# Optimization experiments

Measured on AMD Instinct MI355X. Metric: run time of the kernel, lower is better.

## Reference

```python
import jax, jax.numpy as jnp
import numpy as np
from jax import lax

B, T_IN, N, C_IN = 64, 12, 716, 2
RC = DC = 32      # residual / dilation channels
SC = 8            # skip channels
EC = 512          # end channels
OUT = 12
DIMS = 40
DAYS = 288
TOD = 288
TOPK = 100
DILS = [1, 2, 1, 2, 1, 2, 1, 2]  # blocks=4, layers=2
L = len(DILS)


def setup_inputs() -> dict:
    key = jax.random.key(0)
    ks = iter(jax.random.split(key, 64))
    n = lambda shape, s=0.1: jax.random.normal(next(ks), shape, jnp.float32) * s
    return dict(
        history_data=jax.random.uniform(next(ks), (B, T_IN, N, C_IN), jnp.float32),
        alpha=jnp.float32(-5.0),
        nodevec_p1=n((DAYS, DIMS), 1.0),
        nodevec_p2=n((N, DIMS), 1.0),
        nodevec_p3=n((N, DIMS), 1.0),
        nodevec_pk=n((DIMS, DIMS, DIMS), 1.0),
        pivweight=n((N, N), 1.0),
        start_W=n((RC, 1)), start_b=n((RC,)),
        starta_W=n((1, 1)), starta_b=n((1,)),
        filter_W=n((L, DC, RC, 1, 2)), filter_b=n((L, DC)),
        gate_W=n((L, DC, RC, 1, 2)), gate_b=n((L, DC)),
        skip_W=n((L, SC, DC)), skip_b=n((L, SC)),
        gconv_W=n((L, RC, 3 * DC)), gconv_b=n((L, RC)),
        pgconv_W=n((L, RC, 3 * RC)), pgconv_b=n((L, RC)),
        bn_gamma=jnp.ones((L, RC), jnp.float32),
        bn_beta=jnp.zeros((L, RC), jnp.float32),
        end1_W=n((EC, SC * 52)), end1_b=n((EC,)),
        end2_W=n((OUT, EC)), end2_b=n((OUT,)),
    )


def _conv1x1(x, W, b):  # x [B,C,N,T], W [O,C]
    return jnp.einsum('bcnt,oc->bont', x, W) + b[None, :, None, None]


def _gcn(x, A, W, b):
    # diffusion order 2 over one support; A [B,N,N] or [N,N]
    sub = 'bcvt,bwv->bcwt' if A.ndim == 3 else 'bcvt,wv->bcwt'
    x1 = jnp.einsum(sub, x, A)
    x2 = jnp.einsum(sub, x1, A)
    return _conv1x1(jnp.concatenate([x, x1, x2], axis=1), W, b)


def _forward(history_data, alpha, nodevec_p1, nodevec_p2, nodevec_p3, nodevec_pk,
             pivweight, start_W, start_b, starta_W, starta_b,
             filter_W, filter_b, gate_W, gate_b, skip_W, skip_b,
             gconv_W, gconv_b, pgconv_W, pgconv_b, bn_gamma, bn_beta,
             end1_W, end1_b, end2_W, end2_b):
    inputs = jnp.transpose(history_data[..., 0:1], (0, 3, 2, 1))  # [B,1,N,T]
    inputs = jnp.pad(inputs, ((0, 0), (0, 0), (0, 0), (1, 0)))    # T -> 13 = receptive field
    ind = (history_data[:, -1, 0, 1] * TOD).astype(jnp.int32) % DAYS

    x = _conv1x1(inputs, start_W, start_b)      # [B,RC,N,13]
    x_a = _conv1x1(inputs, starta_W, starta_b)  # [B,1,N,13]

    # dynamic adjacency (dgconstruct)
    adp = jnp.einsum('ai,ijk->ajk', nodevec_p1[ind], nodevec_pk)
    adp = jnp.einsum('bj,ajk->abk', nodevec_p2, adp)
    adp = jnp.einsum('ck,abk->abc', nodevec_p3, adp)
    adj = jax.nn.softmax(jax.nn.relu(adp), axis=2)  # [B,N,N]

    # pivotal adjacency (pivotalconstruct) with top-k node mask
    xs = x_a[:, 0].sum(0)                   # [N,T]
    y = xs.sum(1)[None, :]                  # [1,N]
    adjp = (xs[:, :-1] @ xs[:, 1:].T) / y   # [N,N]
    adjp = adjp * pivweight
    score = adjp.sum(0) + adjp.sum(1)
    _, idx = lax.top_k(score, TOPK)
    mask = jnp.zeros((N,), bool).at[idx].set(True)
    adj_p = jax.nn.softmax(jax.nn.relu(adjp * mask[:, None] * mask[None, :]), axis=1)  # [N,N]

    a_s = jax.nn.sigmoid(alpha)
    dn = ('NCHW', 'OIHW', 'NCHW')
    skip = None
    for i, d in enumerate(DILS):
        residual = x
        filt = jnp.tanh(
            lax.conv_general_dilated(residual, filter_W[i], (1, 1), 'VALID',
                                     rhs_dilation=(1, d), dimension_numbers=dn)
            + filter_b[i][None, :, None, None])
        gate = jax.nn.sigmoid(
            lax.conv_general_dilated(residual, gate_W[i], (1, 1), 'VALID',
                                     rhs_dilation=(1, d), dimension_numbers=dn)
            + gate_b[i][None, :, None, None])
        xg = _gcn(filt * gate, adj, gconv_W[i], gconv_b[i])  # [B,RC,N,T-d]
        # pgcn: diffusion on residual, then causal temporal crop by dilation
        xa = _gcn(residual, adj_p, pgconv_W[i], pgconv_b[i])[..., : residual.shape[3] - d]
        x = a_s * xa + (1.0 - a_s) * xg
        x = x + residual[..., -x.shape[3]:]
        s = _conv1x1(x, skip_W[i], skip_b[i])  # [B,SC,N,Ti]
        s = jnp.transpose(s, (0, 1, 3, 2)).reshape(s.shape[0], -1, s.shape[2], 1)  # [B,SC*Ti,N,1]
        skip = s if skip is None else jnp.concatenate([s, skip], axis=1)
        # BatchNorm2d, train-mode batch stats, fresh affine
        mu = x.mean(axis=(0, 2, 3), keepdims=True)
        var = x.var(axis=(0, 2, 3), keepdims=True)
        x = ((x - mu) / jnp.sqrt(var + 1e-5)) * bn_gamma[i][None, :, None, None] \
            + bn_beta[i][None, :, None, None]

    out = jax.nn.relu(skip)                         # [B,SC*52,N,1]
    out = jax.nn.relu(_conv1x1(out, end1_W, end1_b))
    out = _conv1x1(out, end2_W, end2_b)             # [B,OUT,N,1]
    return out


def reference(history_data, alpha, nodevec_p1, nodevec_p2, nodevec_p3, nodevec_pk,
              pivweight, start_W, start_b, starta_W, starta_b,
              filter_W, filter_b, gate_W, gate_b, skip_W, skip_b,
              gconv_W, gconv_b, pgconv_W, pgconv_b, bn_gamma, bn_beta,
              end1_W, end1_b, end2_W, end2_b):
    return _forward(history_data, alpha, nodevec_p1, nodevec_p2, nodevec_p3, nodevec_pk,
                    pivweight, start_W, start_b, starta_W, starta_b,
                    filter_W, filter_b, gate_W, gate_b, skip_W, skip_b,
                    gconv_W, gconv_b, pgconv_W, pgconv_b, bn_gamma, bn_beta,
                    end1_W, end1_b, end2_W, end2_b)
```

## Files before the change

kernel.cpp:

```cpp
#include <hip/hip_runtime.h>
#include <math.h>

#define NN 716
#define NSQ (716*716)
#define MAXG 9216
#define FPAD 70
#define XPAD 102
typedef unsigned short bfu;
typedef __attribute__((ext_vector_type(8))) __bf16 bf16x8;
typedef __attribute__((ext_vector_type(4))) float f32x4;

__device__ __forceinline__ float b2f(bfu u){ union{unsigned int i; float f;} x; x.i = ((unsigned int)u)<<16; return x.f; }
__device__ __forceinline__ bfu f2b(float f){ union{float fv; unsigned int i;} x; x.fv = f; unsigned int r = (x.i + 0x7fffu + ((x.i>>16)&1u)) >> 16; return (bfu)r; }
__device__ __forceinline__ float sigmoidf_(float x){ return 1.f/(1.f+expf(-x)); }

__device__ __forceinline__ float fexp_(float x){
#if __has_builtin(__builtin_amdgcn_exp2f)
  return __builtin_amdgcn_exp2f(x * 1.44269504088896340736f);
#else
  return __expf(x);
#endif
}
__device__ __forceinline__ float frcp_(float x){
#if __has_builtin(__builtin_amdgcn_rcpf)
  return __builtin_amdgcn_rcpf(x);
#else
  return 1.f/x;
#endif
}
__device__ __forceinline__ float fsig_(float x){ return frcp_(1.f + fexp_(-x)); }
__device__ __forceinline__ float ftanh_(float x){
  float xc = fminf(fmaxf(x, -30.f), 30.f);
  float e = fexp_(-2.f*xc);
  return (1.f - e) * frcp_(1.f + e);
}


__global__ void k_ind(const float* __restrict__ hist, int* __restrict__ ind){
  int b = threadIdx.x; if (b >= 64) return;
  float v = hist[((b*12+11)*NN + 0)*2 + 1];
  ind[b] = ((int)(v*288.0f)) % 288;
}

__global__ void k_dg1(const float* __restrict__ p1, const float* __restrict__ pk,
                      const int* __restrict__ ind, float* __restrict__ tmp1){
  int b = blockIdx.x;
  __shared__ float p1s[40];
  if (threadIdx.x < 40) p1s[threadIdx.x] = p1[ind[b]*40 + threadIdx.x];
  __syncthreads();
  for (int jk = threadIdx.x; jk < 1600; jk += 256){
    float acc = 0.f;
    for (int i = 0; i < 40; ++i) acc += p1s[i]*pk[i*1600 + jk];
    tmp1[b*1600 + jk] = acc;
  }
}

__global__ void k_dg2(const float* __restrict__ p2, const float* __restrict__ tmp1,
                      float* __restrict__ tmp2){
  int b = blockIdx.y;
  __shared__ float ts[1600];
  for (int i = threadIdx.x; i < 1600; i += 256) ts[i] = tmp1[b*1600+i];
  __syncthreads();
  int idx = blockIdx.x*256 + threadIdx.x;
  if (idx >= NN*40) return;
  int n = idx/40, k = idx%40;
  float acc = 0.f;
  for (int j = 0; j < 40; ++j) acc += p2[n*40+j]*ts[j*40+k];
  tmp2[(long)b*NN*40 + idx] = acc;
}

__global__ void k_p3t(const float* __restrict__ p3, float* __restrict__ p3t){
  int v = blockIdx.x*256 + threadIdx.x; if (v >= NN) return;
  for (int k = 0; k < 40; ++k) p3t[k*NN + v] = p3[v*40 + k];
}

__global__ __launch_bounds__(256) void k_adjrow4s(const float* __restrict__ p3t,
    const float* __restrict__ tmp2, unsigned int* __restrict__ topA,
    int* __restrict__ cntA)
{
  int b = blockIdx.y, w0 = blockIdx.x*4, tid = threadIdx.x;
  int wave = tid >> 6, lane = tid & 63;
  __shared__ float t2s[4][40];
  __shared__ float buf[4][720];
  __shared__ float wred[4][4];
  __shared__ float rstat[4];
  __shared__ int pc[4][12];
  for (int i = tid; i < 160; i += 256){
    int r = i/40, k = i%40; int w = w0 + r;
    t2s[r][k] = (w < NN) ? tmp2[((long)b*NN + w)*40 + k] : 0.f;
  }
  __syncthreads();
  float lmax[4] = {0,0,0,0};
  for (int q = 0; q < 3; ++q){
    int v = tid + q*256;
    if (v < NN){
      float a[4] = {0,0,0,0};
      #pragma unroll 8
      for (int k = 0; k < 40; ++k){
        float pv = p3t[k*NN + v];
        #pragma unroll
        for (int r = 0; r < 4; ++r) a[r] += t2s[r][k]*pv;
      }
      #pragma unroll
      for (int r = 0; r < 4; ++r){
        float val = fmaxf(a[r], 0.f);
        buf[r][v] = val;
        lmax[r] = fmaxf(lmax[r], val);
      }
    }
  }
  #pragma unroll
  for (int r = 0; r < 4; ++r){
    float m = lmax[r];
    for (int s = 32; s > 0; s >>= 1) m = fmaxf(m, __shfl_xor(m, s, 64));
    if (lane == 0) wred[r][wave] = m;
  }
  __syncthreads();
  if (tid < 4) rstat[tid] = fmaxf(fmaxf(wred[tid][0], wred[tid][1]), fmaxf(wred[tid][2], wred[tid][3]));
  __syncthreads();
  float lsum[4] = {0,0,0,0};
  for (int q = 0; q < 3; ++q){
    int v = tid + q*256;
    if (v < NN){
      #pragma unroll
      for (int r = 0; r < 4; ++r){
        float e = fexp_(buf[r][v] - rstat[r]);
        buf[r][v] = e;
        lsum[r] += e;
      }
    }
  }
  __syncthreads();
  #pragma unroll
  for (int r = 0; r < 4; ++r){
    float s = lsum[r];
    for (int k = 32; k > 0; k >>= 1) s += __shfl_xor(s, k, 64);
    if (lane == 0) wred[r][wave] = s;
  }
  __syncthreads();
  if (tid < 4) rstat[tid] = frcp_(wred[tid][0] + wred[tid][1] + wred[tid][2] + wred[tid][3]);
  __syncthreads();
  for (int q = 0; q < 3; ++q){
    int v = tid + q*256;
    #pragma unroll
    for (int r = 0; r < 4; ++r){
      float p = (v < NN) ? buf[r][v]*rstat[r] : 0.f;
      unsigned long long m = __ballot(p >= 1e-7f);
      if (lane == 0) pc[r][q*4+wave] = __popcll(m);
    }
  }
  __syncthreads();
  for (int q = 0; q < 3; ++q){
    int v = tid + q*256;
    #pragma unroll
    for (int r = 0; r < 4; ++r){
      float p = (v < NN) ? buf[r][v]*rstat[r] : 0.f;
      bool qual = (p >= 1e-7f);
      unsigned long long m = __ballot(qual);
      int w = w0 + r;
      if (qual && w < NN){
        int base = 0, me = q*4+wave;
        for (int s = 0; s < me; ++s) base += pc[r][s];
        unsigned long long below = (lane == 0) ? 0ull : (m << (64-lane) >> (64-lane));
        int pos = base + __popcll(below);
        if (pos < 16)
          topA[((long)b*NN + w)*16 + pos] = (((unsigned)v)<<16) | (unsigned)f2b(p);
      }
    }
  }
  __syncthreads();
  if (tid < 4){
    int w = w0 + tid;
    if (w < NN){
      int tot = 0;
      for (int s = 0; s < 12; ++s) tot += pc[tid][s];
      cntA[(long)b*NN + w] = (tot < 16) ? tot : 16;
    }
  }
}

__global__ __launch_bounds__(256) void k_zgather2(const bfu* __restrict__ Xg,
    const unsigned int* __restrict__ topA, const int* __restrict__ cntA,
    bfu* __restrict__ Z1g, bfu* __restrict__ Z2g, int M, long sx)
{
  __shared__ bfu rows[4][720];
  __shared__ bfu zrow[4][720];
  int b = blockIdx.y;
  int tid = threadIdx.x, wave = tid >> 6, lane = tid & 63;
  int m = blockIdx.x*4 + wave;
  if (m < M){
    const bfu* xr = Xg + (long)b*sx + (long)m*NN;
    #pragma unroll
    for (int q = 0; q < 12; ++q){
      int v = lane + q*64;
      if (v < NN) rows[wave][v] = xr[v];
    }
  }
  __syncthreads();
  const unsigned int* ta = topA + (long)b*NN*16;
  const int* ca = cntA + (long)b*NN;
  if (m < M){
    bfu* zr = Z1g + (long)b*sx + (long)m*NN;
    #pragma unroll
    for (int q = 0; q < 12; ++q){
      int w = lane + q*64;
      if (w < NN){
        int cnt = ca[w];
        const unsigned int* lst = ta + (long)w*16;
        float acc = 0.f;
        for (int j = 0; j < cnt; ++j){
          unsigned int e = lst[j];
          acc += b2f((bfu)(e & 0xffffu)) * b2f(rows[wave][e >> 16]);
        }
        bfu zv = f2b(acc);
        zr[w] = zv;
        zrow[wave][w] = zv;
      }
    }
  }
  __syncthreads();
  if (m >= M) return;
  bfu* z2r = Z2g + (long)b*sx + (long)m*NN;
  #pragma unroll
  for (int q = 0; q < 12; ++q){
    int w = lane + q*64;
    if (w < NN){
      int cnt = ca[w];
      const unsigned int* lst = ta + (long)w*16;
      float acc = 0.f;
      for (int j = 0; j < cnt; ++j){
        unsigned int e = lst[j];
        acc += b2f((bfu)(e & 0xffffu)) * b2f(zrow[wave][e >> 16]);
      }
      z2r[w] = f2b(acc);
    }
  }
}

__global__ void k_xs(const float* __restrict__ hist, const float* __restrict__ saW,
                     const float* __restrict__ sab, float* __restrict__ xs, float* __restrict__ y){
  int n = blockIdx.x, b = threadIdx.x;
  float w = saW[0], bb = sab[0];
  float ytot = 0.f;
  for (int t = 0; t < 13; ++t){
    float inp = (t == 0) ? 0.f : hist[((b*12 + (t-1))*NN + n)*2];
    float s = inp;
    for (int off = 32; off > 0; off >>= 1) s += __shfl_down(s, off, 64);
    if (b == 0){ float val = w*s + 64.f*bb; xs[n*13+t] = val; ytot += val; }
  }
  if (b == 0) y[n] = ytot;
}

__global__ void k_adjp(const float* __restrict__ xs, const float* __restrict__ y,
                       const float* __restrict__ piv, float* __restrict__ adjp){
  int i = blockIdx.y;
  __shared__ float xi[13];
  if (threadIdx.x < 13) xi[threadIdx.x] = xs[i*13+threadIdx.x];
  __syncthreads();
  int j = blockIdx.x*256 + threadIdx.x;
  if (j >= NN) return;
  float acc = 0.f;
  #pragma unroll
  for (int t = 0; t < 12; ++t) acc += xi[t]*xs[j*13+t+1];
  adjp[(long)i*NN+j] = acc / y[j] * piv[(long)i*NN+j];
}

__global__ void k_score(const float* __restrict__ adjp, float* __restrict__ score){
  int n = blockIdx.x, tid = threadIdx.x;
  float s = 0.f;
  for (int i = tid; i < NN; i += 256) s += adjp[(long)i*NN+n] + adjp[(long)n*NN+i];
  __shared__ float red[256];
  red[tid] = s; __syncthreads();
  for (int k = 128; k > 0; k >>= 1){ if (tid < k) red[tid] += red[tid+k]; __syncthreads(); }
  if (tid == 0) score[n] = red[0];
}

__global__ void k_topk(const float* __restrict__ score, int* __restrict__ mask){
  __shared__ float v[1024];
  __shared__ int ix[1024];
  int tid = threadIdx.x;
  for (int t = tid; t < 1024; t += 256){ v[t] = (t < NN) ? score[t] : -INFINITY; ix[t] = t; }
  __syncthreads();
  for (int k = 2; k <= 1024; k <<= 1){
    for (int j = k >> 1; j > 0; j >>= 1){
      for (int t = tid; t < 1024; t += 256){
        int l = t ^ j;
        if (l > t){
          bool up = ((t & k) == 0);
          bool g = (v[t] > v[l]) || (v[t] == v[l] && ix[t] < ix[l]);
          if (up ? !g : g){
            float tv = v[t]; v[t] = v[l]; v[l] = tv;
            int ti = ix[t]; ix[t] = ix[l]; ix[l] = ti;
          }
        }
      }
      __syncthreads();
    }
  }
  for (int t = tid; t < NN; t += 256) mask[t] = 0;
  __syncthreads();
  if (tid < 100) mask[ix[tid]] = 1;
}

__global__ void k_pivprep(const float* __restrict__ adjp, const int* __restrict__ mask,
                          int* __restrict__ idxk, int* __restrict__ rankv,
                          float* __restrict__ uvec, float* __restrict__ ApkT){
  __shared__ int sidx[100];
  int tid = threadIdx.x;
  if (tid == 0){
    int c = 0;
    for (int i = 0; i < NN; ++i){
      if (mask[i] && c < 100){ sidx[c] = i; idxk[c] = i; rankv[i] = c; ++c; }
      else rankv[i] = -1;
    }
  }
  __syncthreads();
  if (tid < 100){
    int i = sidx[tid];
    const float* row = adjp + (long)i*NN;
    float mx = 0.f;
    for (int k = 0; k < 100; ++k) mx = fmaxf(mx, row[sidx[k]]);
    float sum = 616.f * fexp_(-mx);
    for (int k = 0; k < 100; ++k) sum += fexp_(fmaxf(row[sidx[k]], 0.f) - mx);
    float inv = 1.f/sum;
    uvec[tid] = fexp_(-mx)*inv;
    for (int k = 0; k < 100; ++k)
      ApkT[k*100 + tid] = fexp_(fmaxf(row[sidx[k]], 0.f) - mx)*inv;
  }
}

__global__ void k_init_x(const float* __restrict__ hist, const float* __restrict__ sW,
                         const float* __restrict__ sb, bfu* __restrict__ x){
  int n = blockIdx.x*256 + threadIdx.x; if (n >= NN) return;
  int t = blockIdx.y, b = blockIdx.z;
  float inp = (t == 0) ? 0.f : hist[((b*12 + (t-1))*NN + n)*2];
  #pragma unroll
  for (int c = 0; c < 32; ++c)
    x[((long)(b*32+c)*13 + t)*NN + n] = f2b(sW[c]*inp + sb[c]);
}

__global__ void k_bnid(float* __restrict__ bnp){
  int c = threadIdx.x; if (c >= 32) return;
  bnp[c*2] = 1.f; bnp[c*2+1] = 0.f;
}

__global__ void k_e1perm(const float* __restrict__ W, bfu* __restrict__ Wb){
  int i = blockIdx.x*256 + threadIdx.x;
  if (i >= 512*416) return;
  int e = i/416, kp = i%416;
  const int off2[9] = {0,96,176,248,304,352,384,408,416};
  const int soff[8] = {320,240,168,112,64,32,8,0};
  const int tpl[8]  = {12,10,9,7,6,4,3,1};
  int L = 0;
  #pragma unroll
  for (int q = 0; q < 8; ++q) if (kp >= off2[q+1]) L = q+1;
  int r = kp - off2[L]; int t = r>>3, sc = r&7;
  int k = soff[L] + sc*tpl[L] + t;
  Wb[e*416+kp] = f2b(W[e*416+k]);
}

#define LDST 44

__global__ __launch_bounds__(256) void gemm_mfma(const bfu* __restrict__ Xg,
    const bfu* __restrict__ Ag, bfu* __restrict__ Cg,
    int M, int K, long sx, long sa, long sc,
    const float* __restrict__ bias, int relu_out, int Trow, int Tcomp)
{
  int bx = gridDim.x, by = gridDim.y, nb = gridDim.z;
  int bX = blockIdx.x, bY = blockIdx.y, bZ = blockIdx.z;
  int bpb = bx*by, total = bpb*nb;
  if ((total & 7) == 0 && (nb & 7) == 0){
    int L = bX + bx*(bY + by*bZ);
    int xcd = L & 7, slot = L >> 3;
    bZ = xcd*(nb >> 3) + slot/bpb;
    int inner = slot % bpb;
    bX = inner % bx; bY = inner / bx;
  }
  const bfu* X = Xg + (long)bZ*sx;
  const bfu* A = Ag + (long)bZ*sa;
  bfu*       C = Cg + (long)bZ*sc;
  int m0 = bY*128, n0 = bX*128;
  __shared__ bfu Xs[128*LDST];
  __shared__ bfu As[128*LDST];
  int tid = threadIdx.x;
  int wave = tid >> 6, lane = tid & 63;
  int wm = (wave >> 1)*64, wn = (wave & 1)*64;
  int lr = lane & 15, lg = lane >> 4;
  f32x4 acc[4][4] = {};
  int ldr = tid >> 1, ldk = (tid & 1)*16;
  int mg = m0 + ldr, ng = n0 + ldr;
  int mrow = (Trow == Tcomp) ? mg : (mg/Tcomp)*Trow + (mg%Tcomp);
  const bfu* xrow = X + (long)mrow*K;
  const bfu* arow = A + (long)ng*K;
  for (int k0 = 0; k0 < K; k0 += 32){
    int kk = k0 + ldk;
    ushort4 z4 = {0,0,0,0};
    ushort4 x0=z4,x1=z4,x2=z4,x3=z4, a0=z4,a1=z4,a2=z4,a3=z4;
    if (mg < M){
      if (kk + 16 <= K){
        const ushort4* s = (const ushort4*)(xrow + kk);
        x0=s[0]; x1=s[1]; x2=s[2]; x3=s[3];
      } else {
        bfu tv[16];
        #pragma unroll
        for (int j=0;j<16;++j) tv[j] = (kk+j < K) ? xrow[kk+j] : (bfu)0;
        const ushort4* s = (const ushort4*)tv;
        x0=s[0]; x1=s[1]; x2=s[2]; x3=s[3];
      }
    }
    if (ng < NN){
      if (kk + 16 <= K){
        const ushort4* s = (const ushort4*)(arow + kk);
        a0=s[0]; a1=s[1]; a2=s[2]; a3=s[3];
      } else {
        bfu tv[16];
        #pragma unroll
        for (int j=0;j<16;++j) tv[j] = (kk+j < K) ? arow[kk+j] : (bfu)0;
        const ushort4* s = (const ushort4*)tv;
        a0=s[0]; a1=s[1]; a2=s[2]; a3=s[3];
      }
    }
    ushort4* xd = (ushort4*)&Xs[ldr*LDST + ldk];
    xd[0]=x0; xd[1]=x1; xd[2]=x2; xd[3]=x3;
    ushort4* ad = (ushort4*)&As[ldr*LDST + ldk];
    ad[0]=a0; ad[1]=a1; ad[2]=a2; ad[3]=a3;
    __syncthreads();
    bf16x8 af[4], bfr[4];
    #pragma unroll
    for (int i=0;i<4;++i){
      af[i]  = *(const bf16x8*)&Xs[(wm + i*16 + lr)*LDST + lg*8];
      bfr[i] = *(const bf16x8*)&As[(wn + i*16 + lr)*LDST + lg*8];
    }
    #pragma unroll
    for (int i=0;i<4;++i)
      #pragma unroll
      for (int j=0;j<4;++j)
        acc[i][j] = __builtin_amdgcn_mfma_f32_16x16x32_bf16(af[i], bfr[j], acc[i][j], 0,0,0);
    __syncthreads();
  }
  #pragma unroll
  for (int i=0;i<4;++i){
    #pragma unroll
    for (int r=0;r<4;++r){
      int m = m0 + wm + i*16 + lg*4 + r;
      if (m >= M) continue;
      float bv = bias ? bias[m] : 0.f;
      #pragma unroll
      for (int j=0;j<4;++j){
        int n = n0 + wn + j*16 + lr;
        if (n < NN){
          float v = acc[i][j][r] + bv;
          if (relu_out) v = fmaxf(v, 0.f);
          C[(long)m*NN + n] = f2b(v);
        }
      }
    }
  }
}

__global__ __launch_bounds__(256) void k_fg_mfma(const bfu* __restrict__ x,
    const float* __restrict__ fWl, const float* __restrict__ fbl,
    const float* __restrict__ gWl, const float* __restrict__ gbl,
    const float* __restrict__ bnp, bfu* __restrict__ fg, int T, int Tp, int d)
{
  __shared__ bfu Bsh[128*FPAD];
  __shared__ bfu Ash[64*FPAD];
  __shared__ float bsh[64];
  int tid = threadIdx.x;
  int tot6 = 6*Tp;
  int L = blockIdx.x + 6*(blockIdx.y + Tp*blockIdx.z);
  int xcd = L & 7, slot = L >> 3;
  int b = xcd + ((slot/tot6) << 3);
  int r6 = slot - (slot/tot6)*tot6;
  int t = r6/6, nb6 = r6 - (r6/6)*6;
  int n0 = nb6*128;
  for (int i = tid; i < 4096; i += 256){
    int row = i >> 6, k = i & 63;
    int o = row >> 1, isg = row & 1;
    int tap = k >> 5, c = k & 31;
    const float* W = isg ? gWl : fWl;
    Ash[row*FPAD + k] = f2b(W[(o*32+c)*2 + tap] * bnp[c*2]);
  }
  if (tid < 64){
    int o = tid >> 1, isg = tid & 1;
    const float* W = isg ? gWl : fWl;
    const float* B = isg ? gbl : fbl;
    float s = B[o];
    for (int c = 0; c < 32; ++c)
      s += (W[(o*32+c)*2] + W[(o*32+c)*2+1]) * bnp[c*2+1];
    bsh[tid] = s;
  }
  #pragma unroll
  for (int i = 0; i < 8; ++i){
    int idx = tid + i*256;
    int n4 = (idx & 31)*4;
    int cc = idx >> 5;
    int c = cc & 31, tap = cc >> 5;
    long base = ((long)(b*32+c)*T + t + (tap ? d : 0))*NN + n0 + n4;
    ushort4 v = {0,0,0,0};
    if (n0 + n4 < NN) v = *(const ushort4*)(x + base);
    Bsh[(n4+0)*FPAD + cc] = v.x;
    Bsh[(n4+1)*FPAD + cc] = v.y;
    Bsh[(n4+2)*FPAD + cc] = v.z;
    Bsh[(n4+3)*FPAD + cc] = v.w;
  }
  __syncthreads();
  int wave = tid >> 6, lane = tid & 63;
  int lr = lane & 15, lg = lane >> 4;
  int rowbase = wave*16;
  bf16x8 a0 = *(const bf16x8*)&Ash[(rowbase+lr)*FPAD + lg*8];
  bf16x8 a1 = *(const bf16x8*)&Ash[(rowbase+lr)*FPAD + 32 + lg*8];
  float bf0 = bsh[rowbase + lg*4 + 0];
  float bg0 = bsh[rowbase + lg*4 + 1];
  float bf1 = bsh[rowbase + lg*4 + 2];
  float bg1 = bsh[rowbase + lg*4 + 3];
  int o0 = (rowbase >> 1) + lg*2;
  #pragma unroll
  for (int nt = 0; nt < 8; ++nt){
    bf16x8 b0 = *(const bf16x8*)&Bsh[(nt*16+lr)*FPAD + lg*8];
    bf16x8 b1 = *(const bf16x8*)&Bsh[(nt*16+lr)*FPAD + 32 + lg*8];
    f32x4 acc = {};
    acc = __builtin_amdgcn_mfma_f32_16x16x32_bf16(a0, b0, acc, 0,0,0);
    acc = __builtin_amdgcn_mfma_f32_16x16x32_bf16(a1, b1, acc, 0,0,0);
    int n = n0 + nt*16 + lr;
    if (n < NN){
      float f0 = acc[0] + bf0, g0 = acc[1] + bg0;
      float f1 = acc[2] + bf1, g1 = acc[3] + bg1;
      fg[((long)(b*32+o0)*Tp + t)*NN + n]   = f2b(ftanh_(f0)*fsig_(g0));
      fg[((long)(b*32+o0+1)*Tp + t)*NN + n] = f2b(ftanh_(f1)*fsig_(g1));
    }
  }
}

__global__ __launch_bounds__(256) void k_xgmix_mfma(bfu* __restrict__ F,
    const bfu* __restrict__ z1, const bfu* __restrict__ z2,
    const float* __restrict__ Wl, const float* __restrict__ bl,
    const float* __restrict__ alpha, int Tp)
{
  __shared__ bfu Bsh[128*XPAD];
  __shared__ bfu Ash[32*XPAD];
  __shared__ float bsh[32];
  int tid = threadIdx.x;
  int tot6 = 6*Tp;
  int L = blockIdx.x + 6*(blockIdx.y + Tp*blockIdx.z);
  int xcd = L & 7, slot = L >> 3;
  int b = xcd + ((slot/tot6) << 3);
  int r6 = slot - (slot/tot6)*tot6;
  int t = r6/6, nb6 = r6 - (r6/6)*6;
  int n0 = nb6*128;
  for (int i = tid; i < 3072; i += 256){
    int o = i/96, k = i - o*96;
    Ash[o*XPAD + k] = f2b(Wl[i]);
  }
  if (tid < 32) bsh[tid] = bl[tid];
  #pragma unroll
  for (int i = 0; i < 12; ++i){
    int idx = tid + i*256;
    int cc = idx % 96;
    int n4 = (idx / 96) * 4;
    const bfu* src = (cc < 32) ? F : ((cc < 64) ? z1 : z2);
    int c = cc & 31;
    long base = ((long)(b*32+c)*Tp + t)*NN + n0 + n4;
    ushort4 v = {0,0,0,0};
    if (n0 + n4 < NN) v = *(const ushort4*)(src + base);
    Bsh[(n4+0)*XPAD + cc] = v.x;
    Bsh[(n4+1)*XPAD + cc] = v.y;
    Bsh[(n4+2)*XPAD + cc] = v.z;
    Bsh[(n4+3)*XPAD + cc] = v.w;
  }
  __syncthreads();
  int wave = tid >> 6, lane = tid & 63;
  int lr = lane & 15, lg = lane >> 4;
  int rt = wave & 1;
  int ntb = wave >> 1;
  bf16x8 a0 = *(const bf16x8*)&Ash[(rt*16+lr)*XPAD + 0  + lg*8];
  bf16x8 a1 = *(const bf16x8*)&Ash[(rt*16+lr)*XPAD + 32 + lg*8];
  bf16x8 a2 = *(const bf16x8*)&Ash[(rt*16+lr)*XPAD + 64 + lg*8];
  float oma = 1.f - sigmoidf_(alpha[0]);
  #pragma unroll
  for (int j = 0; j < 4; ++j){
    int nt = ntb + j*2;
    bf16x8 b0 = *(const bf16x8*)&Bsh[(nt*16+lr)*XPAD + 0  + lg*8];
    bf16x8 b1 = *(const bf16x8*)&Bsh[(nt*16+lr)*XPAD + 32 + lg*8];
    bf16x8 b2 = *(const bf16x8*)&Bsh[(nt*16+lr)*XPAD + 64 + lg*8];
    f32x4 acc = {};
    acc = __builtin_amdgcn_mfma_f32_16x16x32_bf16(a0, b0, acc, 0,0,0);
    acc = __builtin_amdgcn_mfma_f32_16x16x32_bf16(a1, b1, acc, 0,0,0);
    acc = __builtin_amdgcn_mfma_f32_16x16x32_bf16(a2, b2, acc, 0,0,0);
    int n = n0 + nt*16 + lr;
    if (n < NN){
      #pragma unroll
      for (int r = 0; r < 4; ++r){
        int o = rt*16 + lg*4 + r;
        F[((long)(b*32+o)*Tp + t)*NN + n] = f2b(oma*(acc[r] + bsh[o]));
      }
    }
  }
}

__global__ __launch_bounds__(256) void k_pgdiff12(const bfu* __restrict__ X,
    float* __restrict__ U1, bfu* __restrict__ Y1k,
    float* __restrict__ U2, bfu* __restrict__ Y2k,
    const int* __restrict__ idxk, const float* __restrict__ uvec,
    const float* __restrict__ ApkT, const float* __restrict__ bnp,
    int M, int Trow, int Tcomp)
{
  __shared__ float xks[4][100];
  __shared__ float yks[4][100];
  int tid = threadIdx.x;
  int g = tid >> 6, lane = tid & 63;
  int m = blockIdx.x*4 + g;
  bool act = (m < M);
  float s = 0.f, sk = 0.f;
  if (act){
    int mrow = (m/Tcomp)*Trow + (m%Tcomp);
    const bfu* xr = X + (long)mrow*NN;
    #pragma unroll
    for (int q = 0; q < 12; ++q){
      int v = lane + q*64;
      if (v < NN) s += b2f(xr[v]);
    }
    for (int o = 32; o; o >>= 1) s += __shfl_xor(s, o, 64);
    #pragma unroll
    for (int q = 0; q < 2; ++q){
      int k = lane + q*64;
      if (k < 100){
        float v = b2f(xr[idxk[k]]);
        xks[g][k] = v;
        sk += v;
      }
    }
    for (int o = 32; o; o >>= 1) sk += __shfl_xor(sk, o, 64);
  }
  __syncthreads();
  float u1val = 0.f, sumY = 0.f;
  if (act){
    int c = (m / Tcomp) & 31;
    float sb = bnp[c*2], bb = bnp[c*2+1];
    u1val = sb*(s*(1.f/716.f)) + bb;
    if (lane == 0) U1[m] = u1val;
    #pragma unroll
    for (int q = 0; q < 2; ++q){
      int r = lane + q*64;
      if (r < 100){
        float acc = uvec[r]*(s - sk);
        for (int k = 0; k < 100; ++k) acc += ApkT[k*100 + r]*xks[g][k];
        bfu yv = f2b(sb*acc + bb);
        Y1k[(long)m*100 + r] = yv;
        float yf = b2f(yv);
        yks[g][r] = yf;
        sumY += yf;
      }
    }
    for (int o = 32; o; o >>= 1) sumY += __shfl_xor(sumY, o, 64);
  }
  __syncthreads();
  if (!act) return;
  float base = 616.f*u1val;
  if (lane == 0) U2[m] = (base + sumY)*(1.f/716.f);
  #pragma unroll
  for (int q = 0; q < 2; ++q){
    int r = lane + q*64;
    if (r < 100){
      float acc = uvec[r]*base;
      for (int k = 0; k < 100; ++k) acc += ApkT[k*100 + r]*yks[g][k];
      Y2k[(long)m*100 + r] = f2b(acc);
    }
  }
}

__global__ __launch_bounds__(256) void k_ymix(const float* __restrict__ U1,
    const float* __restrict__ U2, const bfu* __restrict__ Y1k, const bfu* __restrict__ Y2k,
    const float* __restrict__ pWl, float* __restrict__ V12, float* __restrict__ M12, int Tp)
{
  int t = blockIdx.x, b = blockIdx.y, tid = threadIdx.x;
  __shared__ float w1t[1024], w2t[1024];
  __shared__ float y1s[3200], y2s[3200];
  __shared__ float u1s[32], u2s[32];
  for (int i = tid; i < 1024; i += 256){
    int o = i & 31, c = i >> 5;
    w1t[c*32+o] = pWl[o*96+32+c];
    w2t[c*32+o] = pWl[o*96+64+c];
  }
  for (int i = tid; i < 3200; i += 256){
    int c = i/100, r = i - c*100;
    long m = (long)(b*32+c)*Tp + t;
    y1s[i] = b2f(Y1k[m*100 + r]);
    y2s[i] = b2f(Y2k[m*100 + r]);
  }
  if (tid < 32){
    long m = (long)(b*32+tid)*Tp + t;
    u1s[tid] = U1[m]; u2s[tid] = U2[m];
  }
  __syncthreads();
  for (int i = tid; i < 3200; i += 256){
    int r = i >> 5, o = i & 31;
    float acc = 0.f;
    #pragma unroll 8
    for (int c = 0; c < 32; ++c)
      acc += w1t[c*32+o]*y1s[c*100+r] + w2t[c*32+o]*y2s[c*100+r];
    M12[((long)(b*Tp+t)*100 + r)*32 + o] = acc;
  }
  if (tid < 32){
    float acc = 0.f;
    #pragma unroll 8
    for (int c = 0; c < 32; ++c)
      acc += w1t[c*32+tid]*u1s[c] + w2t[c*32+tid]*u2s[c];
    V12[(long)(b*Tp+t)*32 + tid] = acc;
  }
}

__global__ __launch_bounds__(256) void k_combine3nc(const bfu* __restrict__ x,
    bfu* __restrict__ F, const int* __restrict__ rankv,
    const float* __restrict__ M12, const float* __restrict__ V12,
    const float* __restrict__ pWl, const float* __restrict__ pbl,
    const float* __restrict__ skWl, const float* __restrict__ skbl,
    const float* __restrict__ alpha, const float* __restrict__ bnp,
    bfu* __restrict__ skipP, float* __restrict__ bnred,
    int T, int Tp, int d, int off2)
{
  __shared__ float w0t[1024];
  __shared__ bfu Msb[101*34];
  __shared__ float swt[256], bnl[64], pbs[32], sb8[8];
  int tid = threadIdx.x;
  int tot2 = 2*Tp;
  int L = blockIdx.x + 2*(blockIdx.y + Tp*blockIdx.z);
  int xcd = L & 7, slot = L >> 3;
  int b = xcd + ((slot/tot2) << 3);
  int r2 = slot - (slot/tot2)*tot2;
  int t = r2/2, bx2 = r2 & 1;
  for (int i = tid; i < 1024; i += 256){
    int o = i & 31, c = i >> 5;
    w0t[c*32+o] = pWl[o*96+c];
  }
  for (int i = tid; i < 3434; i += 256){
    int r = i/34, o = i - r*34;
    if (o < 32)
      Msb[r*34+o] = f2b((r < 100) ? M12[((long)(b*Tp+t)*100 + r)*32 + o]
                                  : V12[(long)(b*Tp+t)*32 + o]);
  }
  swt[tid] = skWl[tid];
  if (tid < 64) bnl[tid] = bnp[tid];
  if (tid < 32) pbs[tid] = pbl[tid];
  if (tid < 8)  sb8[tid] = skbl[tid];
  __syncthreads();
  int n = bx2*512 + tid*2;
  bool act = (n < NN);
  float ax[32], ay[32];
  #pragma unroll
  for (int o = 0; o < 32; ++o){ ax[o] = pbs[o]; ay[o] = pbs[o]; }
  const float4* w04 = (const float4*)w0t;
  if (act){
    #pragma unroll 2
    for (int c = 0; c < 32; ++c){
      float sc = bnl[c*2], bc = bnl[c*2+1];
      ushort2 xv = *(const ushort2*)(x + ((long)(b*32+c)*T + t)*NN + n);
      float x0 = b2f(xv.x)*sc + bc;
      float x1 = b2f(xv.y)*sc + bc;
      #pragma unroll
      for (int o4 = 0; o4 < 8; ++o4){
        float4 w = w04[c*8+o4];
        ax[o4*4+0] += w.x*x0;  ay[o4*4+0] += w.x*x1;
        ax[o4*4+1] += w.y*x0;  ay[o4*4+1] += w.y*x1;
        ax[o4*4+2] += w.z*x0;  ay[o4*4+2] += w.z*x1;
        ax[o4*4+3] += w.w*x0;  ay[o4*4+3] += w.w*x1;
      }
    }
  }
  int ra = act ? rankv[n]   : -1;
  int rb = act ? rankv[n+1] : -1;
  int sela = (ra < 0) ? 100 : ra;
  int selb = (rb < 0) ? 100 : rb;
  float a_s = sigmoidf_(alpha[0]);
  #pragma unroll
  for (int o = 0; o < 32; ++o){
    float v0 = 0.f, v1 = 0.f;
    if (act){
      float scb = bnl[o*2], bcb = bnl[o*2+1];
      long oidx = ((long)(b*32+o)*Tp + t)*NN + n;
      ushort2 gv = *(const ushort2*)(F + oidx);
      ushort2 rv = *(const ushort2*)(x + ((long)(b*32+o)*T + t + d)*NN + n);
      v0 = a_s*(ax[o] + b2f(Msb[sela*34+o])) + b2f(gv.x) + b2f(rv.x)*scb + bcb;
      v1 = a_s*(ay[o] + b2f(Msb[selb*34+o])) + b2f(gv.y) + b2f(rv.y)*scb + bcb;
      ushort2 ov; ov.x = f2b(v0); ov.y = f2b(v1);
      *(ushort2*)(F + oidx) = ov;
    }
    ax[o] = v0; ay[o] = v1;
  }
  {
    int wave = tid >> 6;
    int gid = ((blockIdx.x + gridDim.x*(blockIdx.y + gridDim.y*blockIdx.z)) << 2) + wave;
    #pragma unroll
    for (int o = 0; o < 32; ++o){
      float v  = ax[o] + ay[o];
      float vq = ax[o]*ax[o] + ay[o]*ay[o];
      for (int s = 32; s; s >>= 1){
        v  += __shfl_xor(v,  s, 64);
        vq += __shfl_xor(vq, s, 64);
      }
      if ((tid & 63) == 0){
        bnred[((long)o*MAXG + gid)*2]     = v;
        bnred[((long)o*MAXG + gid)*2 + 1] = vq;
      }
    }
  }
  if (!act) return;
  const float4* sw4 = (const float4*)swt;
  #pragma unroll
  for (int sc2 = 0; sc2 < 8; ++sc2){
    float s0 = sb8[sc2], s1 = sb8[sc2];
    #pragma unroll
    for (int c4 = 0; c4 < 8; ++c4){
      float4 w = sw4[sc2*8 + c4];
      s0 += w.x*ax[c4*4] + w.y*ax[c4*4+1] + w.z*ax[c4*4+2] + w.w*ax[c4*4+3];
      s1 += w.x*ay[c4*4] + w.y*ay[c4*4+1] + w.z*ay[c4*4+2] + w.w*ay[c4*4+3];
    }
    ushort2 ov; ov.x = f2b(fmaxf(s0, 0.f)); ov.y = f2b(fmaxf(s1, 0.f));
    *(ushort2*)(skipP + ((long)b*416 + off2 + t*8 + sc2)*NN + n) = ov;
  }
}

__global__ void k_bn2v2(const float* __restrict__ red, const float* __restrict__ gamma,
                        const float* __restrict__ beta, float* __restrict__ bnp,
                        int layer, int Tp, int ngroups){
  int c = blockIdx.x, tid = threadIdx.x;
  float s = 0.f, s2 = 0.f;
  for (int g = tid; g < ngroups; g += 256){
    s  += red[((long)c*MAXG + g)*2];
    s2 += red[((long)c*MAXG + g)*2 + 1];
  }
  __shared__ float rs[256], rs2[256];
  rs[tid] = s; rs2[tid] = s2; __syncthreads();
  for (int k = 128; k > 0; k >>= 1){
    if (tid < k){ rs[tid] += rs[tid+k]; rs2[tid] += rs2[tid+k]; }
    __syncthreads();
  }
  if (tid == 0){
    float cnt = 64.f*Tp*716.f;
    float mu = rs[0]/cnt, var = rs2[0]/cnt - mu*mu;
    float rstd = rsqrtf(var + 1e-5f);
    float ga = gamma[layer*32+c], be = beta[layer*32+c];
    bnp[c*2] = rstd*ga; bnp[c*2+1] = be - mu*rstd*ga;
  }
}


__global__ __launch_bounds__(256) void k_sktr(const bfu* __restrict__ SP, bfu* __restrict__ ST){
  __shared__ bfu tile[64][66];
  int b = blockIdx.z;
  int n0 = blockIdx.x*64, k0 = blockIdx.y*64;
  int tid = threadIdx.x;
  int tr = tid >> 6, tc = tid & 63;
  #pragma unroll
  for (int p = 0; p < 16; ++p){
    int k = k0 + p*4 + tr, n = n0 + tc;
    tile[p*4+tr][tc] = (k < 416 && n < NN) ? SP[((long)b*416 + k)*NN + n] : (bfu)0;
  }
  __syncthreads();
  #pragma unroll
  for (int p = 0; p < 16; ++p){
    int n = n0 + p*4 + tr, k = k0 + tc;
    if (n < NN && k < 416) ST[((long)b*NN + n)*416 + k] = tile[tc][p*4+tr];
  }
}

__global__ __launch_bounds__(256) void k_end2(const bfu* __restrict__ H,
    const float* __restrict__ W2, const float* __restrict__ b2, float* __restrict__ out)
{
  __shared__ float w[12*512];
  for (int i = threadIdx.x; i < 6144; i += 256) w[i] = W2[i];
  __syncthreads();
  int n = blockIdx.x*256 + threadIdx.x; if (n >= NN) return;
  int b = blockIdx.y;
  float acc[12];
  #pragma unroll
  for (int o = 0; o < 12; ++o) acc[o] = b2[o];
  for (int e = 0; e < 512; ++e){
    float h = b2f(H[((long)b*512+e)*NN + n]);
    #pragma unroll
    for (int o = 0; o < 12; ++o) acc[o] += w[o*512+e]*h;
  }
  #pragma unroll
  for (int o = 0; o < 12; ++o) out[((long)b*12+o)*NN + n] = acc[o];
}


extern "C" void kernel_launch(void* const* d_in, const int* in_sizes, int n_in,
                              void* d_out, int out_size, void* d_ws, size_t ws_size,
                              hipStream_t stream)
{
  const float* hist = (const float*)d_in[0];
  const float* alpha = (const float*)d_in[1];
  const float* p1  = (const float*)d_in[2];
  const float* p2  = (const float*)d_in[3];
  const float* p3  = (const float*)d_in[4];
  const float* pk  = (const float*)d_in[5];
  const float* piv = (const float*)d_in[6];
  const float* sW  = (const float*)d_in[7];
  const float* sb  = (const float*)d_in[8];
  const float* saW = (const float*)d_in[9];
  const float* sab = (const float*)d_in[10];
  const float* fW  = (const float*)d_in[11];
  const float* fb  = (const float*)d_in[12];
  const float* gW  = (const float*)d_in[13];
  const float* gb  = (const float*)d_in[14];
  const float* skW = (const float*)d_in[15];
  const float* skb = (const float*)d_in[16];
  const float* gcW = (const float*)d_in[17];
  const float* gcb = (const float*)d_in[18];
  const float* pgW = (const float*)d_in[19];
  const float* pgb = (const float*)d_in[20];
  const float* bng = (const float*)d_in[21];
  const float* bnb = (const float*)d_in[22];
  const float* e1W = (const float*)d_in[23];
  const float* e1b = (const float*)d_in[24];
  const float* e2W = (const float*)d_in[25];
  const float* e2b = (const float*)d_in[26];
  float* out = (float*)d_out;

  char* base = (char*)d_ws;
  size_t off = 0;
  auto alloc = [&](size_t bytes)->char*{
    char* r = base + off;
    off = (off + bytes + 255) & ~(size_t)255;
    return r;
  };
  const size_t SZ12 = 64UL*32*12*716*2;
  const size_t SZ13 = 64UL*32*13*716*2;
  bfu*   t1    = (bfu*)  alloc(SZ12);
  bfu*   t2    = (bfu*)  alloc(SZ12);
  bfu*   P     = (bfu*)  alloc(SZ13);
  bfu*   Q     = (bfu*)  alloc(SZ12);
  bfu*   skipP = (bfu*)  alloc(64UL*416*716*2);
  bfu*   skipT = (bfu*)  alloc(64UL*716*416*2);
  float* adjp  = (float*)alloc((size_t)NSQ*4);
  float* tmp1  = (float*)alloc(64UL*1600*4);
  float* tmp2  = (float*)alloc(64UL*716*40*4);
  float* p3t   = (float*)alloc(40UL*716*4);
  bfu*   e1Wb  = (bfu*)  alloc(512UL*416*2);
  unsigned int* topA = (unsigned int*)alloc(64UL*NN*16*4);
  int*   cntA  = (int*)  alloc(64UL*NN*4);
  float* xs    = (float*)alloc(716UL*13*4);
  float* yv    = (float*)alloc(716UL*4);
  float* score = (float*)alloc(716UL*4);
  float* bnred = (float*)alloc(32UL*MAXG*2*4);
  float* bnp   = (float*)alloc(64UL*4);
  float* bnpid = (float*)alloc(64UL*4);
  float* uvec  = (float*)alloc(100UL*4);
  float* ApkT  = (float*)alloc(100UL*100*4);
  int*   ind   = (int*)  alloc(64UL*4);
  int*   mask  = (int*)  alloc(716UL*4);
  int*   idxk  = (int*)  alloc(100UL*4);
  int*   rankv = (int*)  alloc(716UL*4);

  char* t1c = (char*)t1;
  float* U1  = (float*)(t1c);
  float* U2  = (float*)(t1c +   98304);
  float* V12 = (float*)(t1c + 2*98304);
  float* M12 = (float*)(t1c + 3*98304);
  bfu*   Y1k = (bfu*)  (t1c + 3*98304 + 9830400);
  bfu*   Y2k = (bfu*)  (t1c + 3*98304 + 9830400 + 4915200);

  bfu* hidden = t1;

  k_ind<<<1,64,0,stream>>>(hist, ind);
  k_dg1<<<64,256,0,stream>>>(p1, pk, ind, tmp1);
  k_dg2<<<dim3(112,64),256,0,stream>>>(p2, tmp1, tmp2);
  k_p3t<<<3,256,0,stream>>>(p3, p3t);
  k_adjrow4s<<<dim3(179,64),256,0,stream>>>(p3t, tmp2, topA, cntA);
  k_xs<<<716,64,0,stream>>>(hist, saW, sab, xs, yv);
  k_adjp<<<dim3(3,716),256,0,stream>>>(xs, yv, piv, adjp);
  k_score<<<716,256,0,stream>>>(adjp, score);
  k_topk<<<1,256,0,stream>>>(score, mask);
  k_pivprep<<<1,256,0,stream>>>(adjp, mask, idxk, rankv, uvec, ApkT);
  k_init_x<<<dim3(3,13,64),256,0,stream>>>(hist, sW, sb, P);
  k_e1perm<<<(512*416+255)/256,256,0,stream>>>(e1W, e1Wb);
  k_bnid<<<1,64,0,stream>>>(bnpid);

  int T = 13;
  bfu* x = P;
  bfu* F = Q;
  static const int off2_[8] = {0,96,176,248,304,352,384,408};
  for (int i = 0; i < 8; ++i){
    int d = (i & 1) ? 2 : 1;
    int Tp = T - d;
    const float* bnin = (i == 0) ? bnpid : bnp;
    dim3 g2n(2, Tp, 64);
    dim3 g6(6, Tp, 64);
    k_fg_mfma<<<g6,256,0,stream>>>(x, fW + i*2048, fb + i*32, gW + i*2048, gb + i*32,
        bnin, F, T, Tp, d);
    int M1 = 32*Tp; long sx1 = (long)M1*NN;
    dim3 gz((M1+3)/4, 64);
    k_zgather2<<<gz,256,0,stream>>>(F, topA, cntA, t1, t2, M1, sx1);
    k_xgmix_mfma<<<g6,256,0,stream>>>(F, t1, t2, gcW + i*3072, gcb + i*32, alpha, Tp);
    int M2 = 64*32*Tp;
    k_pgdiff12<<<M2/4,256,0,stream>>>(x, U1, Y1k, U2, Y2k, idxk, uvec, ApkT, bnin,
        M2, T, Tp);
    k_ymix<<<dim3(Tp,64),256,0,stream>>>(U1, U2, Y1k, Y2k, pgW + i*3072, V12, M12, Tp);
    k_combine3nc<<<g2n,256,0,stream>>>(x, F, rankv, M12, V12, pgW + i*3072, pgb + i*32,
        skW + i*256, skb + i*8, alpha, bnin, skipP, bnred, T, Tp, d, off2_[i]);
    int ngroups = 2*Tp*64*4;
    k_bn2v2<<<32,256,0,stream>>>(bnred, bng, bnb, bnp, i, Tp, ngroups);
    bfu* tmp = x; x = F; F = tmp;
    T = Tp;
  }
  k_sktr<<<dim3(12,7,64),256,0,stream>>>(skipP, skipT);
  gemm_mfma<<<dim3(6,4,64),256,0,stream>>>(e1Wb, skipT, hidden, 512, 416,
      0L, 416L*716, 512L*716, e1b, 1, 1, 1);
  k_end2<<<dim3(3,64),256,0,stream>>>(hidden, e2W, e2b, out);
}
```

Before: 2.545 ms.

## Use MFMA for the combine kernel's 32x32 channel mix with LDS-staged tiles

Rewrites the combine kernel so the 32x32 channel projection of the batch-normalised input runs as bf16 MFMA 16x16x32 tiles. The gate, residual and input tiles are staged in LDS with coalesced ushort4 loads, and the grid changes from 2 to 6 node-blocks of 128 nodes. The epilogue then runs on only 128 threads per block, one node each. This adds bf16 rounding of the projection output and leaves half the threads idle in the epilogue, with the BN-reduction group count adjusted to match.

```diff
diff --git a/kernel.cpp b/kernel.cpp
--- a/kernel.cpp
+++ b/kernel.cpp
@@ -6,6 +6,8 @@
 #define MAXG 9216
 #define FPAD 70
 #define XPAD 102
+#define CPAD 40
+#define OPAD 34
 typedef unsigned short bfu;
 typedef __attribute__((ext_vector_type(8))) __bf16 bf16x8;
 typedef __attribute__((ext_vector_type(4))) float f32x4;
@@ -710,7 +712,7 @@
   }
 }
 
-__global__ __launch_bounds__(256) void k_combine3nc(const bfu* __restrict__ x,
+__global__ __launch_bounds__(256) void k_combine_mfma(const bfu* __restrict__ x,
     bfu* __restrict__ F, const int* __restrict__ rankv,
     const float* __restrict__ M12, const float* __restrict__ V12,
     const float* __restrict__ pWl, const float* __restrict__ pbl,
@@ -719,86 +721,110 @@
     bfu* __restrict__ skipP, float* __restrict__ bnred,
     int T, int Tp, int d, int off2)
 {
-  __shared__ float w0t[1024];
-  __shared__ bfu Msb[101*34];
-  __shared__ float swt[256], bnl[64], pbs[32], sb8[8];
+  __shared__ bfu Ash[32*CPAD];
+  __shared__ bfu Bsh[128*CPAD];
+  __shared__ bfu Gsh[128*OPAD];
+  __shared__ bfu Rsh[128*OPAD];
+  __shared__ bfu Osh[128*OPAD];
+  __shared__ bfu Msb[101*OPAD];
+  __shared__ float swt[256], bnl[64], sb8[8];
   int tid = threadIdx.x;
-  int tot2 = 2*Tp;
-  int L = blockIdx.x + 2*(blockIdx.y + Tp*blockIdx.z);
+  int tot6 = 6*Tp;
+  int L = blockIdx.x + 6*(blockIdx.y + Tp*blockIdx.z);
   int xcd = L & 7, slot = L >> 3;
-  int b = xcd + ((slot/tot2) << 3);
-  int r2 = slot - (slot/tot2)*tot2;
-  int t = r2/2, bx2 = r2 & 1;
+  int b = xcd + ((slot/tot6) << 3);
+  int r6 = slot - (slot/tot6)*tot6;
+  int t = r6/6, nb6 = r6 - (r6/6)*6;
+  int n0 = nb6*128;
   for (int i = tid; i < 1024; i += 256){
-    int o = i & 31, c = i >> 5;
-    w0t[c*32+o] = pWl[o*96+c];
-  }
-  for (int i = tid; i < 3434; i += 256){
-    int r = i/34, o = i - r*34;
+    int o = i >> 5, c = i & 31;
+    Ash[o*CPAD + c] = f2b(pWl[o*96 + c]);
+  }
+  if (tid < 64) bnl[tid] = bnp[tid];
+  swt[tid] = skWl[tid];
+  if (tid < 8) sb8[tid] = skbl[tid];
+  #pragma unroll
+  for (int i = 0; i < 4; ++i){
+    int idx = tid + i*256;
+    int n4 = (idx & 31)*4;
+    int c  = idx >> 5;
+    float sc = bnp[c*2], bc = bnp[c*2+1];
+    long base = ((long)(b*32+c)*T + t)*NN + n0 + n4;
+    ushort4 v = {0,0,0,0};
+    if (n0 + n4 < NN) v = *(const ushort4*)(x + base);
+    Bsh[(n4+0)*CPAD + c] = f2b(b2f(v.x)*sc + bc);
+    Bsh[(n4+1)*CPAD + c] = f2b(b2f(v.y)*sc + bc);
+    Bsh[(n4+2)*CPAD + c] = f2b(b2f(v.z)*sc + bc);
+    Bsh[(n4+3)*CPAD + c] = f2b(b2f(v.w)*sc + bc);
+  }
+  #pragma unroll
+  for (int i = 0; i < 4; ++i){
+    int idx = tid + i*256;
+    int n4 = (idx & 31)*4;
+    int o  = idx >> 5;
+    long og  = ((long)(b*32+o)*Tp + t)*NN + n0 + n4;
+    long orr = ((long)(b*32+o)*T + t + d)*NN + n0 + n4;
+    ushort4 g = {0,0,0,0}, r = {0,0,0,0};
+    if (n0 + n4 < NN){ g = *(const ushort4*)(F + og); r = *(const ushort4*)(x + orr); }
+    Gsh[(n4+0)*OPAD+o]=g.x; Gsh[(n4+1)*OPAD+o]=g.y; Gsh[(n4+2)*OPAD+o]=g.z; Gsh[(n4+3)*OPAD+o]=g.w;
+    Rsh[(n4+0)*OPAD+o]=r.x; Rsh[(n4+1)*OPAD+o]=r.y; Rsh[(n4+2)*OPAD+o]=r.z; Rsh[(n4+3)*OPAD+o]=r.w;
+  }
+  for (int i = tid; i < 101*OPAD; i += 256){
+    int r = i/OPAD, o = i - r*OPAD;
     if (o < 32)
-      Msb[r*34+o] = f2b((r < 100) ? M12[((long)(b*Tp+t)*100 + r)*32 + o]
-                                  : V12[(long)(b*Tp+t)*32 + o]);
-  }
-  swt[tid] = skWl[tid];
-  if (tid < 64) bnl[tid] = bnp[tid];
-  if (tid < 32) pbs[tid] = pbl[tid];
-  if (tid < 8)  sb8[tid] = skbl[tid];
-  __syncthreads();
-  int n = bx2*512 + tid*2;
-  bool act = (n < NN);
-  float ax[32], ay[32];
-  #pragma unroll
-  for (int o = 0; o < 32; ++o){ ax[o] = pbs[o]; ay[o] = pbs[o]; }
-  const float4* w04 = (const float4*)w0t;
-  if (act){
-    #pragma unroll 2
-    for (int c = 0; c < 32; ++c){
-      float sc = bnl[c*2], bc = bnl[c*2+1];
-      ushort2 xv = *(const ushort2*)(x + ((long)(b*32+c)*T + t)*NN + n);
-      float x0 = b2f(xv.x)*sc + bc;
-      float x1 = b2f(xv.y)*sc + bc;
+      Msb[r*OPAD+o] = f2b(((r < 100) ? M12[((long)(b*Tp+t)*100 + r)*32 + o]
+                                     : V12[(long)(b*Tp+t)*32 + o]) + pbl[o]);
+  }
+  __syncthreads();
+  {
+    int wave = tid >> 6, lane = tid & 63;
+    int lr = lane & 15, lg = lane >> 4;
+    int rt = wave & 1, ntb = wave >> 1;
+    bf16x8 a0 = *(const bf16x8*)&Ash[(rt*16+lr)*CPAD + lg*8];
+    #pragma unroll
+    for (int j = 0; j < 4; ++j){
+      int nt = ntb + j*2;
+      bf16x8 b0 = *(const bf16x8*)&Bsh[(nt*16+lr)*CPAD + lg*8];
+      f32x4 acc = {};
+      acc = __builtin_amdgcn_mfma_f32_16x16x32_bf16(a0, b0, acc, 0,0,0);
+      int nn = nt*16 + lr;
       #pragma unroll
-      for (int o4 = 0; o4 < 8; ++o4){
-        float4 w = w04[c*8+o4];
-        ax[o4*4+0] += w.x*x0;  ay[o4*4+0] += w.x*x1;
-        ax[o4*4+1] += w.y*x0;  ay[o4*4+1] += w.y*x1;
-        ax[o4*4+2] += w.z*x0;  ay[o4*4+2] += w.z*x1;
-        ax[o4*4+3] += w.w*x0;  ay[o4*4+3] += w.w*x1;
-      }
-    }
-  }
-  int ra = act ? rankv[n]   : -1;
-  int rb = act ? rankv[n+1] : -1;
-  int sela = (ra < 0) ? 100 : ra;
-  int selb = (rb < 0) ? 100 : rb;
+      for (int r = 0; r < 4; ++r){
+        int o = rt*16 + lg*4 + r;
+        Osh[nn*OPAD + o] = f2b(acc[r]);
+      }
+    }
+  }
+  __syncthreads();
+  if (tid >= 128) return;
+  int wave = tid >> 6, lane = tid & 63;
+  int n = tid, gn = n0 + tid;
+  bool act = (gn < NN);
+  int sel = 100;
+  if (act){ int ra = rankv[gn]; sel = (ra < 0) ? 100 : ra; }
   float a_s = sigmoidf_(alpha[0]);
+  float out32[32];
   #pragma unroll
   for (int o = 0; o < 32; ++o){
-    float v0 = 0.f, v1 = 0.f;
+    float val = 0.f;
     if (act){
       float scb = bnl[o*2], bcb = bnl[o*2+1];
-      long oidx = ((long)(b*32+o)*Tp + t)*NN + n;
-      ushort2 gv = *(const ushort2*)(F + oidx);
-      ushort2 rv = *(const ushort2*)(x + ((long)(b*32+o)*T + t + d)*NN + n);
-      v0 = a_s*(ax[o] + b2f(Msb[sela*34+o])) + b2f(gv.x) + b2f(rv.x)*scb + bcb;
-      v1 = a_s*(ay[o] + b2f(Msb[selb*34+o])) + b2f(gv.y) + b2f(rv.y)*scb + bcb;
-      ushort2 ov; ov.x = f2b(v0); ov.y = f2b(v1);
-      *(ushort2*)(F + oidx) = ov;
-    }
-    ax[o] = v0; ay[o] = v1;
+      val = a_s*(b2f(Osh[n*OPAD+o]) + b2f(Msb[sel*OPAD+o]))
+          + b2f(Gsh[n*OPAD+o]) + b2f(Rsh[n*OPAD+o])*scb + bcb;
+      F[((long)(b*32+o)*Tp + t)*NN + gn] = f2b(val);
+    }
+    out32[o] = val;
   }
   {
-    int wave = tid >> 6;
-    int gid = ((blockIdx.x + gridDim.x*(blockIdx.y + gridDim.y*blockIdx.z)) << 2) + wave;
+    int gid = L*2 + wave;
     #pragma unroll
     for (int o = 0; o < 32; ++o){
-      float v  = ax[o] + ay[o];
-      float vq = ax[o]*ax[o] + ay[o]*ay[o];
+      float v = out32[o], vq = out32[o]*out32[o];
       for (int s = 32; s; s >>= 1){
         v  += __shfl_xor(v,  s, 64);
         vq += __shfl_xor(vq, s, 64);
       }
-      if ((tid & 63) == 0){
+      if (lane == 0){
         bnred[((long)o*MAXG + gid)*2]     = v;
         bnred[((long)o*MAXG + gid)*2 + 1] = vq;
       }
@@ -808,15 +834,13 @@
   const float4* sw4 = (const float4*)swt;
   #pragma unroll
   for (int sc2 = 0; sc2 < 8; ++sc2){
-    float s0 = sb8[sc2], s1 = sb8[sc2];
+    float s0 = sb8[sc2];
     #pragma unroll
     for (int c4 = 0; c4 < 8; ++c4){
       float4 w = sw4[sc2*8 + c4];
-      s0 += w.x*ax[c4*4] + w.y*ax[c4*4+1] + w.z*ax[c4*4+2] + w.w*ax[c4*4+3];
-      s1 += w.x*ay[c4*4] + w.y*ay[c4*4+1] + w.z*ay[c4*4+2] + w.w*ay[c4*4+3];
-    }
-    ushort2 ov; ov.x = f2b(fmaxf(s0, 0.f)); ov.y = f2b(fmaxf(s1, 0.f));
-    *(ushort2*)(skipP + ((long)b*416 + off2 + t*8 + sc2)*NN + n) = ov;
+      s0 += w.x*out32[c4*4] + w.y*out32[c4*4+1] + w.z*out32[c4*4+2] + w.w*out32[c4*4+3];
+    }
+    skipP[((long)b*416 + off2 + t*8 + sc2)*NN + gn] = f2b(fmaxf(s0, 0.f));
   }
 }
 
@@ -985,7 +1009,6 @@
     int d = (i & 1) ? 2 : 1;
     int Tp = T - d;
     const float* bnin = (i == 0) ? bnpid : bnp;
-    dim3 g2n(2, Tp, 64);
     dim3 g6(6, Tp, 64);
     k_fg_mfma<<<g6,256,0,stream>>>(x, fW + i*2048, fb + i*32, gW + i*2048, gb + i*32,
         bnin, F, T, Tp, d);
@@ -997,9 +1020,9 @@
     k_pgdiff12<<<M2/4,256,0,stream>>>(x, U1, Y1k, U2, Y2k, idxk, uvec, ApkT, bnin,
         M2, T, Tp);
     k_ymix<<<dim3(Tp,64),256,0,stream>>>(U1, U2, Y1k, Y2k, pgW + i*3072, V12, M12, Tp);
-    k_combine3nc<<<g2n,256,0,stream>>>(x, F, rankv, M12, V12, pgW + i*3072, pgb + i*32,
+    k_combine_mfma<<<g6,256,0,stream>>>(x, F, rankv, M12, V12, pgW + i*3072, pgb + i*32,
         skW + i*256, skb + i*8, alpha, bnin, skipP, bnred, T, Tp, d, off2_[i]);
-    int ngroups = 2*Tp*64*4;
+    int ngroups = 6*Tp*64*2;
     k_bn2v2<<<32,256,0,stream>>>(bnred, bng, bnb, bnp, i, Tp, ngroups);
     bfu* tmp = x; x = F; F = tmp;
     T = Tp;
```

Result: slower. 2.777 ms (+9.1%).
